# Optimization experiments

Measured on AMD Instinct MI355X. Metric: run time of the kernel, lower is better.

Reference implementation:

```python
import jax, jax.numpy as jnp
import numpy as np

LMBDA = 0.1
ALPHA = 0.05
NBIT = 4


def setup_inputs() -> dict:
    key = jax.random.key(0)
    k1, k2 = jax.random.split(key)
    shape = (4096, 16384)
    weight = jax.random.normal(k1, shape, dtype=jnp.float32) * 0.05
    Qn, Qp = -2 ** (NBIT - 1), 2 ** (NBIT - 1) - 1
    q_int = jax.random.randint(k2, shape, Qn, Qp + 1)  # bins in [-8, 7]
    weight_q = (q_int.astype(jnp.float32)) * ALPHA
    alpha = jnp.full((1,), ALPHA, dtype=jnp.float32)
    return {"weight": weight, "weight_q": weight_q, "nbit": NBIT, "alpha": alpha}


def reference(weight, weight_q, nbit, alpha):
    # dampening_loss with aggregation='mean', scaled by lmbda (single quant layer)
    Qn = -2 ** (nbit - 1)
    Qp = 2 ** (nbit - 1) - 1
    nbins = Qp - Qn + 1
    a = alpha.reshape(())

    # (w_q.detach() - w)^2 mean  (detach is a no-op in fwd)
    loss = jnp.mean((weight_q - weight) ** 2)

    # Fused histogram pass: per-bin count / sum / sumsq of `weight`,
    # keyed by the quant bin of weight_q (exact-equality mask in original).
    bin_id = jnp.round(weight_q / a).astype(jnp.int32) - Qn  # [0, nbins)
    w = weight.reshape(-1)
    b = bin_id.reshape(-1)
    cnt = jax.ops.segment_sum(jnp.ones_like(w), b, num_segments=nbins)
    s = jax.ops.segment_sum(w, b, num_segments=nbins)
    ss = jax.ops.segment_sum(w * w, b, num_segments=nbins)

    # unbiased variance per bin, only added when count > 1 (as in torch.var)
    denom_n = jnp.maximum(cnt, 1.0)
    denom_nm1 = jnp.maximum(cnt - 1.0, 1.0)
    var = (ss - s * s / denom_n) / denom_nm1
    loss = loss + jnp.sum(jnp.where(cnt > 1.0, var, 0.0))

    return LMBDA * loss
```

## Files before the change

### kernel.cpp

```cpp
#include <hip/hip_runtime.h>

#define NBINS  16
#define STRIDE 17
#define BLOCKS 768
#define TPB    256


__global__ __launch_bounds__(TPB) void binreg_main(
    const float* __restrict__ w, const float* __restrict__ wq,
    const float* __restrict__ alpha_p, const int* __restrict__ nbit_p,
    float* __restrict__ partial, long long n)
{
    __shared__ float s_pl [TPB * STRIDE];
    __shared__ float ss_pl[TPB * STRIDE];
    __shared__ float c_pl [TPB * STRIDE];
    __shared__ float sqpart[TPB / 64];

    const int tid = threadIdx.x;
    const int tb  = tid * STRIDE;

    #pragma unroll
    for (int k = 0; k < NBINS; ++k) {
        s_pl [tb + k] = 0.0f;
        ss_pl[tb + k] = 0.0f;
        c_pl [tb + k] = 0.0f;
    }

    const float inv_a = 1.0f / alpha_p[0];
    const int   qoff  = 1 << (nbit_p[0] - 1);

    const long long n4     = n >> 2;
    const long long stride = (long long)BLOCKS * TPB;
    const float4* w4 = (const float4*)w;
    const float4* q4 = (const float4*)wq;

    float sq = 0.0f;

    for (long long i = (long long)blockIdx.x * TPB + tid; i < n4; i += stride) {
        float4 a = w4[i];
        float4 b = q4[i];

        float d0 = b.x - a.x, d1 = b.y - a.y, d2 = b.z - a.z, d3 = b.w - a.w;
        sq += d0 * d0 + d1 * d1 + d2 * d2 + d3 * d3;

        int i0 = tb + (((int)rintf(b.x * inv_a) + qoff) & (NBINS - 1));
        int i1 = tb + (((int)rintf(b.y * inv_a) + qoff) & (NBINS - 1));
        int i2 = tb + (((int)rintf(b.z * inv_a) + qoff) & (NBINS - 1));
        int i3 = tb + (((int)rintf(b.w * inv_a) + qoff) & (NBINS - 1));

        c_pl[i0] += 1.0f;  s_pl[i0] += a.x;  ss_pl[i0] += a.x * a.x;
        c_pl[i1] += 1.0f;  s_pl[i1] += a.y;  ss_pl[i1] += a.y * a.y;
        c_pl[i2] += 1.0f;  s_pl[i2] += a.z;  ss_pl[i2] += a.z * a.z;
        c_pl[i3] += 1.0f;  s_pl[i3] += a.w;  ss_pl[i3] += a.w * a.w;
    }

    for (long long i = (n4 << 2) + (long long)blockIdx.x * TPB + tid; i < n; i += stride) {
        float a = w[i], b = wq[i];
        float d = b - a;
        sq += d * d;
        int ii = tb + (((int)rintf(b * inv_a) + qoff) & (NBINS - 1));
        c_pl[ii] += 1.0f;  s_pl[ii] += a;  ss_pl[ii] += a * a;
    }

    for (int off = 32; off; off >>= 1) sq += __shfl_down(sq, off, 64);
    const int wave = tid >> 6, lane = tid & 63;
    if (lane == 0) sqpart[wave] = sq;
    __syncthreads();

    for (int c = wave; c < 48; c += 4) {
        const float* pl = (c < 16) ? c_pl : (c < 32) ? s_pl : ss_pl;
        const int bin = c & 15;
        float v = 0.0f;
        #pragma unroll
        for (int r = 0; r < TPB / 64; ++r)
            v += pl[(r * 64 + lane) * STRIDE + bin];
        for (int off = 32; off; off >>= 1) v += __shfl_down(v, off, 64);
        if (lane == 0) partial[c * BLOCKS + blockIdx.x] = v;
    }
    if (tid == 0)
        partial[48 * BLOCKS + blockIdx.x] =
            sqpart[0] + sqpart[1] + sqpart[2] + sqpart[3];
}

__global__ __launch_bounds__(TPB) void binreg_final(
    const float* __restrict__ partial, float* __restrict__ out, long long n)
{
    __shared__ float cell[49];
    const int tid = threadIdx.x, wave = tid >> 6, lane = tid & 63;

    for (int c = wave; c < 49; c += 4) {
        float v = 0.0f;
        for (int r = lane; r < BLOCKS; r += 64) v += partial[c * BLOCKS + r];
        for (int off = 32; off; off >>= 1) v += __shfl_down(v, off, 64);
        if (lane == 0) cell[c] = v;
    }
    __syncthreads();

    if (tid == 0) {
        float loss = cell[48] / (float)n;
        #pragma unroll
        for (int b = 0; b < NBINS; ++b) {
            float cnt = cell[b];
            float s   = cell[16 + b];
            float ss  = cell[32 + b];
            if (cnt > 1.0f)
                loss += (ss - s * s / cnt) / (cnt - 1.0f);
        }
        out[0] = 0.1f * loss;
    }
}

extern "C" void kernel_launch(void* const* d_in, const int* in_sizes, int n_in,
                              void* d_out, int out_size, void* d_ws, size_t ws_size,
                              hipStream_t stream)
{
    const float* w     = (const float*)d_in[0];
    const float* wq    = (const float*)d_in[1];
    const int*   nbit  = (const int*)d_in[2];
    const float* alpha = (const float*)d_in[3];
    float* out     = (float*)d_out;
    float* partial = (float*)d_ws;
    long long n = (long long)in_sizes[0];

    binreg_main<<<BLOCKS, TPB, 0, stream>>>(w, wq, alpha, nbit, partial, n);
    binreg_final<<<1, TPB, 0, stream>>>(partial, out, n);
}
```

Before: 556.4 us.

## Count bins via wave ballots, shrink shared histogram, prefetch loads, split final reduce

Per-bin counts now come from wave-wide ballot plus popcount into register counters, so shared memory only holds sum and sum-of-squares. Those are stored as bin-major float2 slots, which cuts the shared footprint and allows more blocks per CU (grid raised to 1280, launch bounds set to 5 blocks per CU). The main loop software-prefetches the next float4 pair. The final reduction is split into a 49-block parallel kernel plus a tiny scalar kernel. The cost is 64 ballot/popcount operations per iteration and one extra kernel launch.

```diff
diff --git a/kernel.cpp b/kernel.cpp
--- a/kernel.cpp
+++ b/kernel.cpp
@@ -1,108 +1,145 @@
 #include <hip/hip_runtime.h>
 
-#define NBINS  16
-#define STRIDE 17
-#define BLOCKS 768
-#define TPB    256
+#define NBINS 16
+#define TPB   256
+#define GRID  1280
 
 
-__global__ __launch_bounds__(TPB) void binreg_main(
+__global__ __launch_bounds__(TPB, 5) void binreg_main(
     const float* __restrict__ w, const float* __restrict__ wq,
     const float* __restrict__ alpha_p, const int* __restrict__ nbit_p,
     float* __restrict__ partial, long long n)
 {
-    __shared__ float s_pl [TPB * STRIDE];
-    __shared__ float ss_pl[TPB * STRIDE];
-    __shared__ float c_pl [TPB * STRIDE];
-    __shared__ float sqpart[TPB / 64];
+    __shared__ float2 sv[NBINS * TPB];
 
     const int tid = threadIdx.x;
-    const int tb  = tid * STRIDE;
 
     #pragma unroll
-    for (int k = 0; k < NBINS; ++k) {
-        s_pl [tb + k] = 0.0f;
-        ss_pl[tb + k] = 0.0f;
-        c_pl [tb + k] = 0.0f;
-    }
+    for (int k = 0; k < NBINS; ++k) sv[k * TPB + tid] = make_float2(0.0f, 0.0f);
 
     const float inv_a = 1.0f / alpha_p[0];
     const int   qoff  = 1 << (nbit_p[0] - 1);
 
     const long long n4     = n >> 2;
-    const long long stride = (long long)BLOCKS * TPB;
+    const long long stride = (long long)GRID * TPB;
     const float4* w4 = (const float4*)w;
     const float4* q4 = (const float4*)wq;
 
     float sq = 0.0f;
+    int cnt[NBINS];
+    #pragma unroll
+    for (int k = 0; k < NBINS; ++k) cnt[k] = 0;
 
-    for (long long i = (long long)blockIdx.x * TPB + tid; i < n4; i += stride) {
-        float4 a = w4[i];
-        float4 b = q4[i];
+    long long i = (long long)blockIdx.x * TPB + tid;
+    bool valid = i < n4;
+    float4 a, b;
+    if (valid) { a = w4[i]; b = q4[i]; }
+
+    while (valid) {
+        long long ni = i + stride;
+        bool nvalid = ni < n4;
+        float4 an, bn;
+        if (nvalid) { an = w4[ni]; bn = q4[ni]; }
 
         float d0 = b.x - a.x, d1 = b.y - a.y, d2 = b.z - a.z, d3 = b.w - a.w;
         sq += d0 * d0 + d1 * d1 + d2 * d2 + d3 * d3;
 
-        int i0 = tb + (((int)rintf(b.x * inv_a) + qoff) & (NBINS - 1));
-        int i1 = tb + (((int)rintf(b.y * inv_a) + qoff) & (NBINS - 1));
-        int i2 = tb + (((int)rintf(b.z * inv_a) + qoff) & (NBINS - 1));
-        int i3 = tb + (((int)rintf(b.w * inv_a) + qoff) & (NBINS - 1));
+        int b0 = ((int)rintf(b.x * inv_a) + qoff) & (NBINS - 1);
+        int b1 = ((int)rintf(b.y * inv_a) + qoff) & (NBINS - 1);
+        int b2 = ((int)rintf(b.z * inv_a) + qoff) & (NBINS - 1);
+        int b3 = ((int)rintf(b.w * inv_a) + qoff) & (NBINS - 1);
 
-        c_pl[i0] += 1.0f;  s_pl[i0] += a.x;  ss_pl[i0] += a.x * a.x;
-        c_pl[i1] += 1.0f;  s_pl[i1] += a.y;  ss_pl[i1] += a.y * a.y;
-        c_pl[i2] += 1.0f;  s_pl[i2] += a.z;  ss_pl[i2] += a.z * a.z;
-        c_pl[i3] += 1.0f;  s_pl[i3] += a.w;  ss_pl[i3] += a.w * a.w;
+        #pragma unroll
+        for (int k = 0; k < NBINS; ++k) {
+            cnt[k] += __popcll(__ballot(b0 == k));
+            cnt[k] += __popcll(__ballot(b1 == k));
+            cnt[k] += __popcll(__ballot(b2 == k));
+            cnt[k] += __popcll(__ballot(b3 == k));
+        }
+
+        int i0 = (b0 << 8) + tid;
+        int i1 = (b1 << 8) + tid;
+        int i2 = (b2 << 8) + tid;
+        int i3 = (b3 << 8) + tid;
+
+        { float2 t = sv[i0]; t.x += a.x; t.y += a.x * a.x; sv[i0] = t; }
+        { float2 t = sv[i1]; t.x += a.y; t.y += a.y * a.y; sv[i1] = t; }
+        { float2 t = sv[i2]; t.x += a.z; t.y += a.z * a.z; sv[i2] = t; }
+        { float2 t = sv[i3]; t.x += a.w; t.y += a.w * a.w; sv[i3] = t; }
+
+        i = ni; valid = nvalid; a = an; b = bn;
     }
 
-    for (long long i = (n4 << 2) + (long long)blockIdx.x * TPB + tid; i < n; i += stride) {
-        float a = w[i], b = wq[i];
-        float d = b - a;
+    for (long long t4 = (n4 << 2) + (long long)blockIdx.x * TPB + tid; t4 < n; t4 += stride) {
+        float av = w[t4], bv = wq[t4];
+        float d = bv - av;
         sq += d * d;
-        int ii = tb + (((int)rintf(b * inv_a) + qoff) & (NBINS - 1));
-        c_pl[ii] += 1.0f;  s_pl[ii] += a;  ss_pl[ii] += a * a;
+        int bb = ((int)rintf(bv * inv_a) + qoff) & (NBINS - 1);
+        #pragma unroll
+        for (int k = 0; k < NBINS; ++k) cnt[k] += __popcll(__ballot(bb == k));
+        int ii = (bb << 8) + tid;
+        float2 t = sv[ii]; t.x += av; t.y += av * av; sv[ii] = t;
     }
 
     for (int off = 32; off; off >>= 1) sq += __shfl_down(sq, off, 64);
     const int wave = tid >> 6, lane = tid & 63;
-    if (lane == 0) sqpart[wave] = sq;
     __syncthreads();
 
-    for (int c = wave; c < 48; c += 4) {
-        const float* pl = (c < 16) ? c_pl : (c < 32) ? s_pl : ss_pl;
+    for (int c = wave; c < 32; c += 4) {
         const int bin = c & 15;
         float v = 0.0f;
         #pragma unroll
-        for (int r = 0; r < TPB / 64; ++r)
-            v += pl[(r * 64 + lane) * STRIDE + bin];
+        for (int r = 0; r < TPB / 64; ++r) {
+            float2 t = sv[(bin << 8) + r * 64 + lane];
+            v += (c < 16) ? t.x : t.y;
+        }
         for (int off = 32; off; off >>= 1) v += __shfl_down(v, off, 64);
-        if (lane == 0) partial[c * BLOCKS + blockIdx.x] = v;
-    }
-    if (tid == 0)
-        partial[48 * BLOCKS + blockIdx.x] =
-            sqpart[0] + sqpart[1] + sqpart[2] + sqpart[3];
-}
-
-__global__ __launch_bounds__(TPB) void binreg_final(
-    const float* __restrict__ partial, float* __restrict__ out, long long n)
-{
-    __shared__ float cell[49];
-    const int tid = threadIdx.x, wave = tid >> 6, lane = tid & 63;
-
-    for (int c = wave; c < 49; c += 4) {
-        float v = 0.0f;
-        for (int r = lane; r < BLOCKS; r += 64) v += partial[c * BLOCKS + r];
-        for (int off = 32; off; off >>= 1) v += __shfl_down(v, off, 64);
-        if (lane == 0) cell[c] = v;
+        if (lane == 0) partial[c * GRID + blockIdx.x] = v;
     }
     __syncthreads();
 
-    if (tid == 0) {
-        float loss = cell[48] / (float)n;
+    float* stage = (float*)sv;
+    if (lane == 0) {
+        #pragma unroll
+        for (int k = 0; k < NBINS; ++k) stage[wave * NBINS + k] = (float)cnt[k];
+        stage[64 + wave] = sq;
+    }
+    __syncthreads();
+
+    if (tid < NBINS) {
+        float v = stage[tid] + stage[16 + tid] + stage[32 + tid] + stage[48 + tid];
+        partial[(32 + tid) * GRID + blockIdx.x] = v;
+    }
+    if (tid == 16)
+        partial[48 * GRID + blockIdx.x] =
+            (stage[64] + stage[65]) + (stage[66] + stage[67]);
+}
+
+__global__ __launch_bounds__(TPB) void binreg_final1(
+    const float* __restrict__ partial, float* __restrict__ cells)
+{
+    const int c = blockIdx.x;
+    const int tid = threadIdx.x, wave = tid >> 6, lane = tid & 63;
+    __shared__ float wsum[4];
+
+    float v = 0.0f;
+    for (int r = tid; r < GRID; r += TPB) v += partial[c * GRID + r];
+    for (int off = 32; off; off >>= 1) v += __shfl_down(v, off, 64);
+    if (lane == 0) wsum[wave] = v;
+    __syncthreads();
+    if (tid == 0) cells[c] = (wsum[0] + wsum[1]) + (wsum[2] + wsum[3]);
+}
+
+__global__ void binreg_final2(const float* __restrict__ cells,
+                              float* __restrict__ out, long long n)
+{
+    if (threadIdx.x == 0 && blockIdx.x == 0) {
+        float loss = cells[48] / (float)n;
         #pragma unroll
         for (int b = 0; b < NBINS; ++b) {
-            float cnt = cell[b];
-            float s   = cell[16 + b];
-            float ss  = cell[32 + b];
+            float s   = cells[b];
+            float ss  = cells[16 + b];
+            float cnt = cells[32 + b];
             if (cnt > 1.0f)
                 loss += (ss - s * s / cnt) / (cnt - 1.0f);
         }
@@ -120,8 +157,10 @@
     const float* alpha = (const float*)d_in[3];
     float* out     = (float*)d_out;
     float* partial = (float*)d_ws;
+    float* cells   = partial + 49 * GRID;
     long long n = (long long)in_sizes[0];
 
-    binreg_main<<<BLOCKS, TPB, 0, stream>>>(w, wq, alpha, nbit, partial, n);
-    binreg_final<<<1, TPB, 0, stream>>>(partial, out, n);
+    binreg_main  <<<GRID, TPB, 0, stream>>>(w, wq, alpha, nbit, partial, n);
+    binreg_final1<<<49,   TPB, 0, stream>>>(partial, cells);
+    binreg_final2<<<1,    64,  0, stream>>>(cells, out, n);
 }
```

After: 569.8 us. +2.4%, slower.
